# Kernel optimization log

Hardware: AMD Instinct MI355X
Metric: run time of the kernel (lower is better)

The kernel has to match this reference:

```python
import jax, jax.numpy as jnp
import numpy as np

K = 5       # kernel_size
NV = 12     # number of orientation vectors
CIN = 8
COUT = 8

ICO = np.array([[-0.525731, 0.850651, 0.0], [0.525731, 0.850651, 0.0],
                [-0.525731, -0.850651, 0.0], [0.525731, -0.850651, 0.0],
                [0.0, -0.525731, 0.850651], [0.0, 0.525731, 0.850651],
                [0.0, -0.525731, -0.850651], [0.0, 0.525731, -0.850651],
                [0.850651, 0.0, -0.525731], [0.850651, 0.0, 0.525731],
                [-0.850651, 0.0, -0.525731], [-0.850651, 0.0, 0.525731]],
               dtype=np.float32)


def _attrs():
    # invariant_attr_r3s2_fiber_bundle on the fixed k^3 stencil graph
    off = np.arange(K) - K // 2 + (K + 1) % 2 * 0.5
    grid = np.stack(np.meshgrid(off, off, off, indexing='ij'), 0)
    pos = grid.transpose(1, 2, 3, 0).reshape(-1, 3)              # [K^3, 3]
    rel = pos[K ** 3 // 2][None, :] - pos                        # pos_send - pos_receive, [E,3]
    inv1 = (rel[:, None, :] * ICO[None]).sum(-1, keepdims=True)  # [E,NV,1] parallel component
    inv2 = np.linalg.norm(rel[:, None, :] - inv1 * ICO[None], axis=-1, keepdims=True)  # orthogonal norm
    spatial = np.concatenate([inv1, inv2], -1).round(5).reshape(-1, 2)   # rounded as in module
    spherical = (ICO @ ICO.T).round(3).reshape(-1, 1)                     # [NV*NV, 1]
    return jnp.asarray(spatial, jnp.float32), jnp.asarray(spherical, jnp.float32)


def _poly(x, degree=3):
    # PolynomialFeatures: cat of x, x(x)x, x(x)x(x)x flattened
    feats = [x]
    for _ in range(1, degree):
        f = feats[-1][..., :, None] * x[..., None, :]
        feats.append(f.reshape(f.shape[:-2] + (-1,)))
    return jnp.concatenate(feats, -1)


def _mlp(a, w1, b1, w2, b2, w3):
    h = jax.nn.gelu(a @ w1.T + b1, approximate=False)
    h = jax.nn.gelu(h @ w2.T + b2, approximate=False)
    return h @ w3.T


def setup_inputs() -> dict:
    key = jax.random.key(0)
    ks = jax.random.split(key, 8)
    spatial, spherical = _attrs()

    def lin(k, o, i):
        return (jax.random.normal(k, (o, i), jnp.float32) / np.sqrt(i)).astype(jnp.float32)

    return dict(
        x=jax.random.normal(ks[0], (2, CIN, NV, 64, 64, 64), jnp.float32),
        spatial_attr=spatial,            # [1500, 2]
        spherical_attr=spherical,        # [144, 1]
        basis_w1=lin(ks[1], 8, 14), basis_b1=jnp.zeros(8, jnp.float32),
        basis_w2=lin(ks[2], 8, 8),  basis_b2=jnp.zeros(8, jnp.float32),
        basis_w3=lin(ks[3], CIN, 8),
        fiber_w1=lin(ks[4], 8, 3),  fiber_b1=jnp.zeros(8, jnp.float32),
        fiber_w2=lin(ks[5], 8, 8),  fiber_b2=jnp.zeros(8, jnp.float32),
        fiber_w3=lin(ks[6], CIN * COUT, 8),
        bias=jnp.full((1, COUT, 1, 1, 1, 1), 0.01, jnp.float32),
    )


def reference(x, spatial_attr, spherical_attr,
              basis_w1, basis_b1, basis_w2, basis_b2, basis_w3,
              fiber_w1, fiber_b1, fiber_w2, fiber_b2, fiber_w3, bias):
    # Spatial (depthwise) kernel generated by tiny MLP on edge invariants.
    # (Original uniques attrs then gathers; basis(unique)[inverse] == basis(attr), so apply directly.)
    sw = _mlp(_poly(spatial_attr), basis_w1, basis_b1, basis_w2, basis_b2, basis_w3)  # [K^3*NV, CIN]
    sw = sw.reshape(K, K, K, NV, CIN).transpose(4, 3, 0, 1, 2).reshape(CIN * NV, 1, K, K, K)
    # Fiber (orientation-mixing) weights from MLP on orientation invariants.
    fw = _mlp(_poly(spherical_attr), fiber_w1, fiber_b1, fiber_w2, fiber_b2, fiber_w3)  # [NV*NV, CIN*COUT]
    fw = fw.reshape(NV, NV, CIN, COUT).transpose(3, 2, 0, 1)  # [COUT, CIN, NV, NV]

    B, _, _, X, Y, Z = x.shape
    xr = x.reshape(B, CIN * NV, X, Y, Z)
    y = jax.lax.conv_general_dilated(
        xr, sw, window_strides=(1, 1, 1), padding='SAME',
        feature_group_count=CIN * NV,
        dimension_numbers=('NCDHW', 'OIDHW', 'NCDHW'))
    y = y.reshape(B, CIN, NV, X, Y, Z)
    out = jnp.einsum('bfvxyz,gfvw->bgwxyz', y, fw)
    return out + bias
```

## Files before the change

### kernel.cpp

```cpp
#include <hip/hip_runtime.h>
#include <math.h>

#define DEV __device__ __forceinline__

DEV float gelu_exact(float v) {
    return 0.5f * v * (1.0f + erff(v * 0.7071067811865476f));
}

typedef __attribute__((ext_vector_type(8))) short bf16x8;
typedef __attribute__((ext_vector_type(4))) float f32x4;

DEV short f2b(float f) {
    unsigned u = __builtin_bit_cast(unsigned, f);
    unsigned r = (u + 0x7fffu + ((u >> 16) & 1u)) >> 16;
    return (short)r;
}

__global__ __launch_bounds__(256) void wk(
    const float* __restrict__ spatial, const float* __restrict__ spherical,
    const float* __restrict__ bw1, const float* __restrict__ bb1,
    const float* __restrict__ bw2, const float* __restrict__ bb2,
    const float* __restrict__ bw3,
    const float* __restrict__ fw1, const float* __restrict__ fb1,
    const float* __restrict__ fw2, const float* __restrict__ fb2,
    const float* __restrict__ fw3,
    float* __restrict__ sw, float* __restrict__ Mt) {
    const int i = blockIdx.x * 256 + threadIdx.x;
    if (i < 1500) {
        const float a = spatial[2 * i], b = spatial[2 * i + 1];
        float ft[14];
        ft[0] = a; ft[1] = b;
        ft[2] = a * a; ft[3] = a * b; ft[4] = b * a; ft[5] = b * b;
#pragma unroll
        for (int k = 0; k < 4; ++k) {
            ft[6 + 2 * k] = ft[2 + k] * a;
            ft[7 + 2 * k] = ft[2 + k] * b;
        }
        float h1[8], h2[8];
#pragma unroll
        for (int j = 0; j < 8; ++j) {
            float s = bb1[j];
#pragma unroll
            for (int k = 0; k < 14; ++k) s = fmaf(bw1[j * 14 + k], ft[k], s);
            h1[j] = gelu_exact(s);
        }
#pragma unroll
        for (int j = 0; j < 8; ++j) {
            float s = bb2[j];
#pragma unroll
            for (int k = 0; k < 8; ++k) s = fmaf(bw2[j * 8 + k], h1[k], s);
            h2[j] = gelu_exact(s);
        }
        const int o = i / 12, v = i % 12;
#pragma unroll
        for (int c = 0; c < 8; ++c) {
            float s = 0.f;
#pragma unroll
            for (int k = 0; k < 8; ++k) s = fmaf(bw3[c * 8 + k], h2[k], s);
            sw[(c * 12 + v) * 125 + o] = s;
        }
    } else if (i < 1644) {
        const int r = i - 1500;
        const float s0 = spherical[r];
        float ft[3];
        ft[0] = s0; ft[1] = s0 * s0; ft[2] = s0 * s0 * s0;
        float h1[8], h2[8];
#pragma unroll
        for (int j = 0; j < 8; ++j) {
            float s = fb1[j];
#pragma unroll
            for (int k = 0; k < 3; ++k) s = fmaf(fw1[j * 3 + k], ft[k], s);
            h1[j] = gelu_exact(s);
        }
#pragma unroll
        for (int j = 0; j < 8; ++j) {
            float s = fb2[j];
#pragma unroll
            for (int k = 0; k < 8; ++k) s = fmaf(fw2[j * 8 + k], h1[k], s);
            h2[j] = gelu_exact(s);
        }
        const int v = r / 12, w = r % 12;
#pragma unroll
        for (int c = 0; c < 64; ++c) {
            float s = 0.f;
#pragma unroll
            for (int k = 0; k < 8; ++k) s = fmaf(fw3[c * 8 + k], h2[k], s);
            const int f = c >> 3, g = c & 7;
            Mt[(f * 12 + v) * 96 + g * 12 + w] = s;
        }
    }
}

__global__ __launch_bounds__(256) void ck(const float* __restrict__ x,
                                          const float* __restrict__ sw,
                                          float* __restrict__ y) {
    const int ch = blockIdx.y, b = blockIdx.z;
    const int ty = (blockIdx.x & 7) << 3;
    const int tz = (blockIdx.x >> 3) << 3;
    const int t = threadIdx.x;
    const int xq = t & 15, x0 = xq << 2;
    const int y0 = ty + (((t >> 4) & 3) << 1);
    const int z0 = tz + ((t >> 6) << 1);
    const long cb = (long)(b * 96 + ch) << 18;
    const float* __restrict__ xb = x + cb;
    float* __restrict__ yb = y + cb;
    const float* __restrict__ w = sw + ch * 125;

    float acc[2][2][4];
#pragma unroll
    for (int i = 0; i < 2; ++i)
#pragma unroll
        for (int j = 0; j < 2; ++j)
#pragma unroll
            for (int k = 0; k < 4; ++k) acc[i][j][k] = 0.f;

#pragma unroll
    for (int hz = 0; hz < 6; ++hz) {
        const int zz = z0 + hz - 2;
        if (zz < 0 || zz >= 64) continue;
#pragma unroll
        for (int hy = 0; hy < 6; ++hy) {
            const int yy = y0 + hy - 2;
            if (yy >= 0 && yy < 64) {
                const float* row = xb + (zz << 12) + (yy << 6);
                const float4 v4 = *(const float4*)(row + x0);
                const float uz = __shfl_up(v4.z, 1, 16);
                const float uw = __shfl_up(v4.w, 1, 16);
                const float dx_ = __shfl_down(v4.x, 1, 16);
                const float dy_ = __shfl_down(v4.y, 1, 16);
                float f[8];
                f[0] = (xq > 0) ? uz : 0.f;
                f[1] = (xq > 0) ? uw : 0.f;
                f[2] = v4.x; f[3] = v4.y; f[4] = v4.z; f[5] = v4.w;
                f[6] = (xq < 15) ? dx_ : 0.f;
                f[7] = (xq < 15) ? dy_ : 0.f;
#pragma unroll
                for (int dz = 0; dz < 2; ++dz) {
                    const int A = hz - dz;
                    if (A < 0 || A > 4) continue;
#pragma unroll
                    for (int dy = 0; dy < 2; ++dy) {
                        const int B = hy - dy;
                        if (B < 0 || B > 4) continue;
                        const float* wr = w + (A * 5 + B) * 5;
#pragma unroll
                        for (int C = 0; C < 5; ++C) {
                            const float wv = wr[C];
#pragma unroll
                            for (int dx = 0; dx < 4; ++dx)
                                acc[dz][dy][dx] = fmaf(f[C + dx], wv, acc[dz][dy][dx]);
                        }
                    }
                }
            }
        }
    }
#pragma unroll
    for (int dz = 0; dz < 2; ++dz)
#pragma unroll
        for (int dy = 0; dy < 2; ++dy) {
            float4 o;
            o.x = acc[dz][dy][0]; o.y = acc[dz][dy][1];
            o.z = acc[dz][dy][2]; o.w = acc[dz][dy][3];
            *(float4*)(yb + ((z0 + dz) << 12) + ((y0 + dy) << 6) + x0) = o;
        }
}

__global__ __launch_bounds__(256) void ek(float* __restrict__ io,
                                          const float* __restrict__ Mt,
                                          const float* __restrict__ bias) {
    const int t = threadIdx.x;
    const int lane = t & 63;
    const int wv = t >> 6;
    const int l15 = lane & 15, quad = lane >> 4;
    const long b_off = ((long)blockIdx.y * 96) << 18;
    const int pt0 = (blockIdx.x << 7) + (wv << 5);

    bf16x8 Af[6][3];
#pragma unroll
    for (int mt = 0; mt < 6; ++mt)
#pragma unroll
        for (int ks = 0; ks < 3; ++ks)
#pragma unroll
            for (int j = 0; j < 8; ++j) {
                const int fv = ks * 32 + quad * 8 + j;
                Af[mt][ks][j] = f2b(Mt[fv * 96 + mt * 16 + l15]);
            }

    bf16x8 Bf[2][3];
#pragma unroll
    for (int nt = 0; nt < 2; ++nt)
#pragma unroll
        for (int ks = 0; ks < 3; ++ks)
#pragma unroll
            for (int j = 0; j < 8; ++j) {
                const int fv = ks * 32 + quad * 8 + j;
                Bf[nt][ks][j] = f2b(io[b_off + ((long)fv << 18) + pt0 + nt * 16 + l15]);
            }

#pragma unroll
    for (int mt = 0; mt < 6; ++mt)
#pragma unroll
        for (int nt = 0; nt < 2; ++nt) {
            f32x4 c = {0.f, 0.f, 0.f, 0.f};
#pragma unroll
            for (int ks = 0; ks < 3; ++ks)
                c = __builtin_amdgcn_mfma_f32_16x16x32_bf16(Af[mt][ks], Bf[nt][ks], c, 0, 0, 0);
#pragma unroll
            for (int r = 0; r < 4; ++r) {
                const int gw = mt * 16 + quad * 4 + r;
                io[b_off + ((long)gw << 18) + pt0 + nt * 16 + l15] = c[r] + bias[gw / 12];
            }
        }
}

extern "C" void kernel_launch(void* const* d_in, const int* in_sizes, int n_in,
                              void* d_out, int out_size, void* d_ws, size_t ws_size,
                              hipStream_t stream) {
    const float* x        = (const float*)d_in[0];
    const float* spatial  = (const float*)d_in[1];
    const float* spherical= (const float*)d_in[2];
    const float* bw1 = (const float*)d_in[3];
    const float* bb1 = (const float*)d_in[4];
    const float* bw2 = (const float*)d_in[5];
    const float* bb2 = (const float*)d_in[6];
    const float* bw3 = (const float*)d_in[7];
    const float* fw1 = (const float*)d_in[8];
    const float* fb1 = (const float*)d_in[9];
    const float* fw2 = (const float*)d_in[10];
    const float* fb2 = (const float*)d_in[11];
    const float* fw3 = (const float*)d_in[12];
    const float* bias = (const float*)d_in[13];

    float* sw = (float*)d_ws;
    float* Mt = (float*)d_ws + 12032;
    float* out = (float*)d_out;

    hipLaunchKernelGGL(wk, dim3(7), dim3(256), 0, stream,
                       spatial, spherical, bw1, bb1, bw2, bb2, bw3,
                       fw1, fb1, fw2, fb2, fw3, sw, Mt);
    hipLaunchKernelGGL(ck, dim3(64, 96, 2), dim3(256), 0, stream, x, sw, out);
    hipLaunchKernelGGL(ek, dim3(2048, 2, 1), dim3(256), 0, stream, out, Mt, bias);
    (void)in_sizes; (void)n_in; (void)out_size; (void)ws_size;
}
```

Measured before the change: 623.2 us.

## Stage conv halo tile and einsum input in LDS, pre-pack bf16 fiber weights

The depthwise conv kernel now loads a 12x12-row halo tile into shared memory with zero padding and an XOR swizzle. Each thread then computes 8 x-outputs across 2 y rows from LDS, replacing the repeated global loads and cross-lane shuffles. The einsum kernel first stages its 96x128 input slice in LDS with coalesced float4 loads. The fiber weight matrix is pre-transposed and pre-converted to bf16 in the weight kernel, so A fragments become single vector loads per mt. The cost is larger LDS use per block, which may lower occupancy.

```diff
diff --git a/kernel.cpp b/kernel.cpp
--- a/kernel.cpp
+++ b/kernel.cpp
@@ -24,7 +24,7 @@
     const float* __restrict__ fw1, const float* __restrict__ fb1,
     const float* __restrict__ fw2, const float* __restrict__ fb2,
     const float* __restrict__ fw3,
-    float* __restrict__ sw, float* __restrict__ Mt) {
+    float* __restrict__ sw, unsigned short* __restrict__ Mtt) {
     const int i = blockIdx.x * 256 + threadIdx.x;
     if (i < 1500) {
         const float a = spatial[2 * i], b = spatial[2 * i + 1];
@@ -86,132 +86,163 @@
 #pragma unroll
             for (int k = 0; k < 8; ++k) s = fmaf(fw3[c * 8 + k], h2[k], s);
             const int f = c >> 3, g = c & 7;
-            Mt[(f * 12 + v) * 96 + g * 12 + w] = s;
-        }
-    }
-}
-
+            Mtt[(g * 12 + w) * 96 + f * 12 + v] = (unsigned short)f2b(s);
+        }
+    }
+}
+
+#define CPITCH 80
 __global__ __launch_bounds__(256) void ck(const float* __restrict__ x,
                                           const float* __restrict__ sw,
                                           float* __restrict__ y) {
+    __shared__ float lds[12 * 12 * CPITCH];
     const int ch = blockIdx.y, b = blockIdx.z;
     const int ty = (blockIdx.x & 7) << 3;
     const int tz = (blockIdx.x >> 3) << 3;
     const int t = threadIdx.x;
-    const int xq = t & 15, x0 = xq << 2;
-    const int y0 = ty + (((t >> 4) & 3) << 1);
-    const int z0 = tz + ((t >> 6) << 1);
     const long cb = (long)(b * 96 + ch) << 18;
     const float* __restrict__ xb = x + cb;
     float* __restrict__ yb = y + cb;
     const float* __restrict__ w = sw + ch * 125;
 
-    float acc[2][2][4];
+    {
+        const int l16 = t & 15;
+        const int rq = t >> 4;
+#pragma unroll
+        for (int pass = 0; pass < 9; ++pass) {
+            const int r = rq + (pass << 4);
+            const int zi = r / 12, yi = r % 12;
+            const int zz = tz + zi - 2, yy = ty + yi - 2;
+            float4 v = {0.f, 0.f, 0.f, 0.f};
+            if (zz >= 0 && zz < 64 && yy >= 0 && yy < 64)
+                v = *(const float4*)(xb + (zz << 12) + (yy << 6) + (l16 << 2));
+            const int s = (r >> 2) & 3;
+            float* rp = lds + r * CPITCH;
+            float* p0 = rp + (((l16 ^ s) << 2) + 2);
+            p0[0] = v.x; p0[1] = v.y;
+            float* p1 = rp + (((l16 + 1) ^ s) << 2);
+            p1[0] = v.z; p1[1] = v.w;
+            if (l16 == 0) {
+                float* p = rp + ((0 ^ s) << 2);
+                p[0] = 0.f; p[1] = 0.f;
+            }
+            if (l16 == 15) {
+                float* p = rp + (((16 ^ s) << 2) + 2);
+                p[0] = 0.f; p[1] = 0.f;
+            }
+        }
+    }
+    __syncthreads();
+
+    const int xg = t & 7;
+    const int yg = (t >> 3) & 3;
+    const int zg = t >> 5;
+    const int w0 = xg << 1;
+
+    float acc[2][8];
 #pragma unroll
     for (int i = 0; i < 2; ++i)
 #pragma unroll
-        for (int j = 0; j < 2; ++j)
-#pragma unroll
-            for (int k = 0; k < 4; ++k) acc[i][j][k] = 0.f;
-
-#pragma unroll
-    for (int hz = 0; hz < 6; ++hz) {
-        const int zz = z0 + hz - 2;
-        if (zz < 0 || zz >= 64) continue;
+        for (int j = 0; j < 8; ++j) acc[i][j] = 0.f;
+
+#pragma unroll
+    for (int hz = 0; hz < 5; ++hz) {
 #pragma unroll
         for (int hy = 0; hy < 6; ++hy) {
-            const int yy = y0 + hy - 2;
-            if (yy >= 0 && yy < 64) {
-                const float* row = xb + (zz << 12) + (yy << 6);
-                const float4 v4 = *(const float4*)(row + x0);
-                const float uz = __shfl_up(v4.z, 1, 16);
-                const float uw = __shfl_up(v4.w, 1, 16);
-                const float dx_ = __shfl_down(v4.x, 1, 16);
-                const float dy_ = __shfl_down(v4.y, 1, 16);
-                float f[8];
-                f[0] = (xq > 0) ? uz : 0.f;
-                f[1] = (xq > 0) ? uw : 0.f;
-                f[2] = v4.x; f[3] = v4.y; f[4] = v4.z; f[5] = v4.w;
-                f[6] = (xq < 15) ? dx_ : 0.f;
-                f[7] = (xq < 15) ? dy_ : 0.f;
-#pragma unroll
-                for (int dz = 0; dz < 2; ++dz) {
-                    const int A = hz - dz;
-                    if (A < 0 || A > 4) continue;
-#pragma unroll
-                    for (int dy = 0; dy < 2; ++dy) {
-                        const int B = hy - dy;
-                        if (B < 0 || B > 4) continue;
-                        const float* wr = w + (A * 5 + B) * 5;
-#pragma unroll
-                        for (int C = 0; C < 5; ++C) {
-                            const float wv = wr[C];
-#pragma unroll
-                            for (int dx = 0; dx < 4; ++dx)
-                                acc[dz][dy][dx] = fmaf(f[C + dx], wv, acc[dz][dy][dx]);
-                        }
-                    }
+            const int row = (zg + hz) * 12 + (yg << 1) + hy;
+            const int s = (row >> 2) & 3;
+            const float* rp = lds + row * CPITCH;
+            const float4 fa = *(const float4*)(rp + (((w0 + 0) ^ s) << 2));
+            const float4 fb = *(const float4*)(rp + (((w0 + 1) ^ s) << 2));
+            const float4 fc = *(const float4*)(rp + (((w0 + 2) ^ s) << 2));
+            const float f[12] = {fa.x, fa.y, fa.z, fa.w, fb.x, fb.y, fb.z, fb.w,
+                                 fc.x, fc.y, fc.z, fc.w};
+#pragma unroll
+            for (int dy = 0; dy < 2; ++dy) {
+                const int B = hy - dy;
+                if (B < 0 || B > 4) continue;
+                const float* wr = w + (hz * 5 + B) * 5;
+#pragma unroll
+                for (int C = 0; C < 5; ++C) {
+                    const float wv = wr[C];
+#pragma unroll
+                    for (int dx = 0; dx < 8; ++dx)
+                        acc[dy][dx] = fmaf(f[C + dx], wv, acc[dy][dx]);
                 }
             }
         }
     }
-#pragma unroll
-    for (int dz = 0; dz < 2; ++dz)
-#pragma unroll
-        for (int dy = 0; dy < 2; ++dy) {
-            float4 o;
-            o.x = acc[dz][dy][0]; o.y = acc[dz][dy][1];
-            o.z = acc[dz][dy][2]; o.w = acc[dz][dy][3];
-            *(float4*)(yb + ((z0 + dz) << 12) + ((y0 + dy) << 6) + x0) = o;
-        }
-}
-
+
+    const int zo = tz + zg;
+    const int xo = xg << 3;
+#pragma unroll
+    for (int dy = 0; dy < 2; ++dy) {
+        const int yo = ty + (yg << 1) + dy;
+        float* op = yb + (zo << 12) + (yo << 6) + xo;
+        float4 o0 = {acc[dy][0], acc[dy][1], acc[dy][2], acc[dy][3]};
+        float4 o1 = {acc[dy][4], acc[dy][5], acc[dy][6], acc[dy][7]};
+        *(float4*)(op) = o0;
+        *(float4*)(op + 4) = o1;
+    }
+}
+
+#define EPITCH 132
 __global__ __launch_bounds__(256) void ek(float* __restrict__ io,
-                                          const float* __restrict__ Mt,
+                                          const unsigned short* __restrict__ Mtt,
                                           const float* __restrict__ bias) {
+    __shared__ float yt[96 * EPITCH];
     const int t = threadIdx.x;
+    const long b_off = ((long)blockIdx.y * 96) << 18;
+    const int pt0 = blockIdx.x << 7;
+
+    {
+        const int l32 = t & 31;
+        const int r8 = t >> 5;
+#pragma unroll
+        for (int pass = 0; pass < 12; ++pass) {
+            const int fv = r8 + (pass << 3);
+            const float4 v = *(const float4*)(io + b_off + ((long)fv << 18) + pt0 + (l32 << 2));
+            *(float4*)(yt + fv * EPITCH + (l32 << 2)) = v;
+        }
+    }
+    __syncthreads();
+
     const int lane = t & 63;
     const int wv = t >> 6;
     const int l15 = lane & 15, quad = lane >> 4;
-    const long b_off = ((long)blockIdx.y * 96) << 18;
-    const int pt0 = (blockIdx.x << 7) + (wv << 5);
-
-    bf16x8 Af[6][3];
-#pragma unroll
-    for (int mt = 0; mt < 6; ++mt)
+    const int ptl = wv << 5;
+
+    bf16x8 Bf[2][3];
+#pragma unroll
+    for (int nt = 0; nt < 2; ++nt)
 #pragma unroll
         for (int ks = 0; ks < 3; ++ks)
 #pragma unroll
             for (int j = 0; j < 8; ++j) {
                 const int fv = ks * 32 + quad * 8 + j;
-                Af[mt][ks][j] = f2b(Mt[fv * 96 + mt * 16 + l15]);
-            }
-
-    bf16x8 Bf[2][3];
-#pragma unroll
-    for (int nt = 0; nt < 2; ++nt)
+                Bf[nt][ks][j] = f2b(yt[fv * EPITCH + ptl + nt * 16 + l15]);
+            }
+
+    const long po = b_off + pt0 + ptl;
+#pragma unroll
+    for (int mt = 0; mt < 6; ++mt) {
+        bf16x8 Af[3];
 #pragma unroll
         for (int ks = 0; ks < 3; ++ks)
-#pragma unroll
-            for (int j = 0; j < 8; ++j) {
-                const int fv = ks * 32 + quad * 8 + j;
-                Bf[nt][ks][j] = f2b(io[b_off + ((long)fv << 18) + pt0 + nt * 16 + l15]);
-            }
-
-#pragma unroll
-    for (int mt = 0; mt < 6; ++mt)
+            Af[ks] = *(const bf16x8*)(Mtt + (mt * 16 + l15) * 96 + ks * 32 + quad * 8);
 #pragma unroll
         for (int nt = 0; nt < 2; ++nt) {
             f32x4 c = {0.f, 0.f, 0.f, 0.f};
 #pragma unroll
             for (int ks = 0; ks < 3; ++ks)
-                c = __builtin_amdgcn_mfma_f32_16x16x32_bf16(Af[mt][ks], Bf[nt][ks], c, 0, 0, 0);
+                c = __builtin_amdgcn_mfma_f32_16x16x32_bf16(Af[ks], Bf[nt][ks], c, 0, 0, 0);
 #pragma unroll
             for (int r = 0; r < 4; ++r) {
                 const int gw = mt * 16 + quad * 4 + r;
-                io[b_off + ((long)gw << 18) + pt0 + nt * 16 + l15] = c[r] + bias[gw / 12];
-            }
-        }
+                io[po + ((long)gw << 18) + nt * 16 + l15] = c[r] + bias[gw / 12];
+            }
+        }
+    }
 }
 
 extern "C" void kernel_launch(void* const* d_in, const int* in_sizes, int n_in,
@@ -233,13 +264,13 @@
     const float* bias = (const float*)d_in[13];
 
     float* sw = (float*)d_ws;
-    float* Mt = (float*)d_ws + 12032;
+    unsigned short* Mtt = (unsigned short*)((char*)d_ws + 48128);
     float* out = (float*)d_out;
 
     hipLaunchKernelGGL(wk, dim3(7), dim3(256), 0, stream,
                        spatial, spherical, bw1, bb1, bw2, bb2, bw3,
-                       fw1, fb1, fw2, fb2, fw3, sw, Mt);
+                       fw1, fb1, fw2, fb2, fw3, sw, Mtt);
     hipLaunchKernelGGL(ck, dim3(64, 96, 2), dim3(256), 0, stream, x, sw, out);
-    hipLaunchKernelGGL(ek, dim3(2048, 2, 1), dim3(256), 0, stream, out, Mt, bias);
+    hipLaunchKernelGGL(ek, dim3(2048, 2, 1), dim3(256), 0, stream, out, Mtt, bias);
     (void)in_sizes; (void)n_in; (void)out_size; (void)ws_size;
 }
```

Result: faster. 587.1 us (-5.8%).

## Store conv intermediate as packed bf16 and stage mixing GEMM through LDS

Applied to the files above, without the earlier changes.

The depthwise conv kernel now handles two channels per thread and writes its result as packed bf16 pairs instead of fp32. This halves the intermediate write and read traffic. The mixing kernel loads these packed rows into swizzled LDS with coalesced 16-byte accesses, builds the MFMA B fragments from LDS, and writes output through LDS so global stores are fully coalesced. The fiber weights are precomputed as transposed bf16, so the mixing kernel loads A fragments as vectors instead of converting scalars per element. It adds LDS use and barriers, and relies on in-place reuse of the output buffer.

```diff
diff --git a/kernel.cpp b/kernel.cpp
--- a/kernel.cpp
+++ b/kernel.cpp
@@ -24,7 +24,7 @@
     const float* __restrict__ fw1, const float* __restrict__ fb1,
     const float* __restrict__ fw2, const float* __restrict__ fb2,
     const float* __restrict__ fw3,
-    float* __restrict__ sw, float* __restrict__ Mt) {
+    float* __restrict__ sw, unsigned short* __restrict__ Mtt) {
     const int i = blockIdx.x * 256 + threadIdx.x;
     if (i < 1500) {
         const float a = spatial[2 * i], b = spatial[2 * i + 1];
@@ -86,132 +86,193 @@
 #pragma unroll
             for (int k = 0; k < 8; ++k) s = fmaf(fw3[c * 8 + k], h2[k], s);
             const int f = c >> 3, g = c & 7;
-            Mt[(f * 12 + v) * 96 + g * 12 + w] = s;
+            Mtt[(g * 12 + w) * 96 + f * 12 + v] = (unsigned short)f2b(s);
         }
     }
 }
 
 __global__ __launch_bounds__(256) void ck(const float* __restrict__ x,
                                           const float* __restrict__ sw,
-                                          float* __restrict__ y) {
-    const int ch = blockIdx.y, b = blockIdx.z;
+                                          unsigned int* __restrict__ yp) {
+    const int chp = blockIdx.y, b = blockIdx.z;
     const int ty = (blockIdx.x & 7) << 3;
     const int tz = (blockIdx.x >> 3) << 3;
     const int t = threadIdx.x;
     const int xq = t & 15, x0 = xq << 2;
     const int y0 = ty + (((t >> 4) & 3) << 1);
     const int z0 = tz + ((t >> 6) << 1);
-    const long cb = (long)(b * 96 + ch) << 18;
-    const float* __restrict__ xb = x + cb;
-    float* __restrict__ yb = y + cb;
-    const float* __restrict__ w = sw + ch * 125;
-
-    float acc[2][2][4];
-#pragma unroll
-    for (int i = 0; i < 2; ++i)
-#pragma unroll
-        for (int j = 0; j < 2; ++j)
-#pragma unroll
-            for (int k = 0; k < 4; ++k) acc[i][j][k] = 0.f;
-
-#pragma unroll
-    for (int hz = 0; hz < 6; ++hz) {
-        const int zz = z0 + hz - 2;
-        if (zz < 0 || zz >= 64) continue;
-#pragma unroll
-        for (int hy = 0; hy < 6; ++hy) {
-            const int yy = y0 + hy - 2;
-            if (yy >= 0 && yy < 64) {
-                const float* row = xb + (zz << 12) + (yy << 6);
-                const float4 v4 = *(const float4*)(row + x0);
-                const float uz = __shfl_up(v4.z, 1, 16);
-                const float uw = __shfl_up(v4.w, 1, 16);
-                const float dx_ = __shfl_down(v4.x, 1, 16);
-                const float dy_ = __shfl_down(v4.y, 1, 16);
-                float f[8];
-                f[0] = (xq > 0) ? uz : 0.f;
-                f[1] = (xq > 0) ? uw : 0.f;
-                f[2] = v4.x; f[3] = v4.y; f[4] = v4.z; f[5] = v4.w;
-                f[6] = (xq < 15) ? dx_ : 0.f;
-                f[7] = (xq < 15) ? dy_ : 0.f;
-#pragma unroll
-                for (int dz = 0; dz < 2; ++dz) {
-                    const int A = hz - dz;
-                    if (A < 0 || A > 4) continue;
-#pragma unroll
-                    for (int dy = 0; dy < 2; ++dy) {
-                        const int B = hy - dy;
-                        if (B < 0 || B > 4) continue;
-                        const float* wr = w + (A * 5 + B) * 5;
-#pragma unroll
-                        for (int C = 0; C < 5; ++C) {
-                            const float wv = wr[C];
-#pragma unroll
-                            for (int dx = 0; dx < 4; ++dx)
-                                acc[dz][dy][dx] = fmaf(f[C + dx], wv, acc[dz][dy][dx]);
+
+    unsigned int pk[2][2][4];
+
+#pragma unroll
+    for (int c2 = 0; c2 < 2; ++c2) {
+        const int ch = 2 * chp + c2;
+        const float* __restrict__ xb = x + ((long)(b * 96 + ch) << 18);
+        const float* __restrict__ w = sw + ch * 125;
+
+        float acc[2][2][4];
+#pragma unroll
+        for (int i = 0; i < 2; ++i)
+#pragma unroll
+            for (int j = 0; j < 2; ++j)
+#pragma unroll
+                for (int k = 0; k < 4; ++k) acc[i][j][k] = 0.f;
+
+#pragma unroll
+        for (int hz = 0; hz < 6; ++hz) {
+            const int zz = z0 + hz - 2;
+            if (zz < 0 || zz >= 64) continue;
+#pragma unroll
+            for (int hy = 0; hy < 6; ++hy) {
+                const int yy = y0 + hy - 2;
+                if (yy >= 0 && yy < 64) {
+                    const float* row = xb + (zz << 12) + (yy << 6);
+                    const float4 v4 = *(const float4*)(row + x0);
+                    const float uz = __shfl_up(v4.z, 1, 16);
+                    const float uw = __shfl_up(v4.w, 1, 16);
+                    const float dx_ = __shfl_down(v4.x, 1, 16);
+                    const float dy_ = __shfl_down(v4.y, 1, 16);
+                    float f[8];
+                    f[0] = (xq > 0) ? uz : 0.f;
+                    f[1] = (xq > 0) ? uw : 0.f;
+                    f[2] = v4.x; f[3] = v4.y; f[4] = v4.z; f[5] = v4.w;
+                    f[6] = (xq < 15) ? dx_ : 0.f;
+                    f[7] = (xq < 15) ? dy_ : 0.f;
+#pragma unroll
+                    for (int dz = 0; dz < 2; ++dz) {
+                        const int A = hz - dz;
+                        if (A < 0 || A > 4) continue;
+#pragma unroll
+                        for (int dy = 0; dy < 2; ++dy) {
+                            const int B = hy - dy;
+                            if (B < 0 || B > 4) continue;
+                            const float* wr = w + (A * 5 + B) * 5;
+#pragma unroll
+                            for (int C = 0; C < 5; ++C) {
+                                const float wv = wr[C];
+#pragma unroll
+                                for (int dx = 0; dx < 4; ++dx)
+                                    acc[dz][dy][dx] = fmaf(f[C + dx], wv, acc[dz][dy][dx]);
+                            }
                         }
                     }
                 }
             }
         }
-    }
+#pragma unroll
+        for (int dz = 0; dz < 2; ++dz)
+#pragma unroll
+            for (int dy = 0; dy < 2; ++dy)
+#pragma unroll
+                for (int dx = 0; dx < 4; ++dx) {
+                    const unsigned int h = (unsigned short)f2b(acc[dz][dy][dx]);
+                    if (c2 == 0) pk[dz][dy][dx] = h;
+                    else         pk[dz][dy][dx] |= (h << 16);
+                }
+    }
+
+    unsigned int* yb = yp + ((long)(b * 96 + chp) << 18);
 #pragma unroll
     for (int dz = 0; dz < 2; ++dz)
 #pragma unroll
         for (int dy = 0; dy < 2; ++dy) {
-            float4 o;
-            o.x = acc[dz][dy][0]; o.y = acc[dz][dy][1];
-            o.z = acc[dz][dy][2]; o.w = acc[dz][dy][3];
-            *(float4*)(yb + ((z0 + dz) << 12) + ((y0 + dy) << 6) + x0) = o;
+            uint4 o;
+            o.x = pk[dz][dy][0]; o.y = pk[dz][dy][1];
+            o.z = pk[dz][dy][2]; o.w = pk[dz][dy][3];
+            *(uint4*)(yb + ((z0 + dz) << 12) + ((y0 + dy) << 6) + x0) = o;
         }
 }
 
 __global__ __launch_bounds__(256) void ek(float* __restrict__ io,
-                                          const float* __restrict__ Mt,
+                                          const unsigned int* __restrict__ yp,
+                                          const unsigned short* __restrict__ Mtt,
                                           const float* __restrict__ bias) {
+    __shared__ float lds[96 * 128];
+    unsigned int* ldu = (unsigned int*)lds;
     const int t = threadIdx.x;
+    const long row0 = (long)blockIdx.y * 96;
+    const int pt0 = blockIdx.x << 7;
+
+    {
+        const int l32 = t & 31, r8 = t >> 5;
+#pragma unroll
+        for (int pass = 0; pass < 6; ++pass) {
+            const int pr = r8 + (pass << 3);
+            const uint4 v = *(const uint4*)(yp + ((row0 + pr) << 18) + pt0 + (l32 << 2));
+            const int ws = (l32 + pr) & 31;
+            *(uint4*)(ldu + (pr << 7) + (ws << 2)) = v;
+        }
+    }
+    __syncthreads();
+
     const int lane = t & 63;
-    const int wv = t >> 6;
+    const int wv4 = t >> 6;
     const int l15 = lane & 15, quad = lane >> 4;
-    const long b_off = ((long)blockIdx.y * 96) << 18;
-    const int pt0 = (blockIdx.x << 7) + (wv << 5);
-
-    bf16x8 Af[6][3];
-#pragma unroll
-    for (int mt = 0; mt < 6; ++mt)
+    const int ptl = wv4 << 5;
+
+    bf16x8 Bf[2][3];
+#pragma unroll
+    for (int nt = 0; nt < 2; ++nt)
+#pragma unroll
+        for (int ks = 0; ks < 3; ++ks) {
+            const int pt = ptl + nt * 16 + l15;
+            const int pr0 = 16 * ks + 4 * quad;
+            uint4 d;
+            {
+                const int b0 = (pt >> 2) + pr0;
+                d.x = ldu[((pr0 + 0) << 7) + (((b0 + 0) & 31) << 2) + (pt & 3)];
+                d.y = ldu[((pr0 + 1) << 7) + (((b0 + 1) & 31) << 2) + (pt & 3)];
+                d.z = ldu[((pr0 + 2) << 7) + (((b0 + 2) & 31) << 2) + (pt & 3)];
+                d.w = ldu[((pr0 + 3) << 7) + (((b0 + 3) & 31) << 2) + (pt & 3)];
+            }
+            Bf[nt][ks] = __builtin_bit_cast(bf16x8, d);
+        }
+
+    float cv[6][2][4];
+#pragma unroll
+    for (int mt = 0; mt < 6; ++mt) {
+        bf16x8 Af[3];
 #pragma unroll
         for (int ks = 0; ks < 3; ++ks)
-#pragma unroll
-            for (int j = 0; j < 8; ++j) {
-                const int fv = ks * 32 + quad * 8 + j;
-                Af[mt][ks][j] = f2b(Mt[fv * 96 + mt * 16 + l15]);
-            }
-
-    bf16x8 Bf[2][3];
-#pragma unroll
-    for (int nt = 0; nt < 2; ++nt)
-#pragma unroll
-        for (int ks = 0; ks < 3; ++ks)
-#pragma unroll
-            for (int j = 0; j < 8; ++j) {
-                const int fv = ks * 32 + quad * 8 + j;
-                Bf[nt][ks][j] = f2b(io[b_off + ((long)fv << 18) + pt0 + nt * 16 + l15]);
-            }
-
-#pragma unroll
-    for (int mt = 0; mt < 6; ++mt)
+            Af[ks] = *(const bf16x8*)(Mtt + (mt * 16 + l15) * 96 + ks * 32 + quad * 8);
 #pragma unroll
         for (int nt = 0; nt < 2; ++nt) {
             f32x4 c = {0.f, 0.f, 0.f, 0.f};
 #pragma unroll
             for (int ks = 0; ks < 3; ++ks)
-                c = __builtin_amdgcn_mfma_f32_16x16x32_bf16(Af[mt][ks], Bf[nt][ks], c, 0, 0, 0);
+                c = __builtin_amdgcn_mfma_f32_16x16x32_bf16(Af[ks], Bf[nt][ks], c, 0, 0, 0);
+#pragma unroll
+            for (int r = 0; r < 4; ++r) cv[mt][nt][r] = c[r];
+        }
+    }
+    __syncthreads();
+
+#pragma unroll
+    for (int mt = 0; mt < 6; ++mt)
+#pragma unroll
+        for (int nt = 0; nt < 2; ++nt) {
+            const int pt = ptl + nt * 16 + l15;
 #pragma unroll
             for (int r = 0; r < 4; ++r) {
                 const int gw = mt * 16 + quad * 4 + r;
-                io[b_off + ((long)gw << 18) + pt0 + nt * 16 + l15] = c[r] + bias[gw / 12];
+                const int ws = ((pt >> 2) + 2 * (gw >> 2)) & 31;
+                lds[(gw << 7) + (ws << 2) + (pt & 3)] = cv[mt][nt][r];
             }
         }
+    __syncthreads();
+
+    {
+        const int l32 = t & 31, r8 = t >> 5;
+#pragma unroll
+        for (int pass = 0; pass < 12; ++pass) {
+            const int row = r8 + (pass << 3);
+            const int ws = (l32 + 2 * (row >> 2)) & 31;
+            float4 v = *(const float4*)(lds + (row << 7) + (ws << 2));
+            const float bs = bias[row / 12];
+            v.x += bs; v.y += bs; v.z += bs; v.w += bs;
+            *(float4*)(io + ((row0 + row) << 18) + pt0 + (l32 << 2)) = v;
+        }
+    }
 }
 
 extern "C" void kernel_launch(void* const* d_in, const int* in_sizes, int n_in,
@@ -233,13 +294,15 @@
     const float* bias = (const float*)d_in[13];
 
     float* sw = (float*)d_ws;
-    float* Mt = (float*)d_ws + 12032;
+    unsigned short* Mtt = (unsigned short*)((char*)d_ws + 48128);
     float* out = (float*)d_out;
 
     hipLaunchKernelGGL(wk, dim3(7), dim3(256), 0, stream,
                        spatial, spherical, bw1, bb1, bw2, bb2, bw3,
-                       fw1, fb1, fw2, fb2, fw3, sw, Mt);
-    hipLaunchKernelGGL(ck, dim3(64, 96, 2), dim3(256), 0, stream, x, sw, out);
-    hipLaunchKernelGGL(ek, dim3(2048, 2, 1), dim3(256), 0, stream, out, Mt, bias);
+                       fw1, fb1, fw2, fb2, fw3, sw, Mtt);
+    hipLaunchKernelGGL(ck, dim3(64, 48, 2), dim3(256), 0, stream,
+                       x, sw, (unsigned int*)out);
+    hipLaunchKernelGGL(ek, dim3(2048, 2, 1), dim3(256), 0, stream,
+                       out, (const unsigned int*)out, Mtt, bias);
     (void)in_sizes; (void)n_in; (void)out_size; (void)ws_size;
 }
```

Measured after the change: 581.9 us. 1.07x faster.

## Fuse depthwise conv and fiber-mixing MFMA into one kernel via LDS

Applied to the files above, without the earlier changes.

The depthwise 5x5x5 conv and the orientation-mixing GEMM are merged into one kernel. Each block computes conv outputs for all 96 channels of a 4-row tile, packs them as bf16 into swizzled shared memory, and then runs the MFMA mixing directly from LDS. The fiber weights are also precomputed as transposed bf16 so they load as vectors. This removes the full fp32 intermediate round trip through global memory. In exchange each thread computes only 4 outputs per channel, so halo reloads of x increase (25 rows per output row instead of sharing across a 2x2 tile), and LDS use limits occupancy.

```diff
diff --git a/kernel.cpp b/kernel.cpp
--- a/kernel.cpp
+++ b/kernel.cpp
@@ -15,6 +15,8 @@
     unsigned r = (u + 0x7fffu + ((u >> 16) & 1u)) >> 16;
     return (short)r;
 }
+
+DEV int rmap(int pt) { return pt ^ ((pt >> 2) & 7); }
 
 __global__ __launch_bounds__(256) void wk(
     const float* __restrict__ spatial, const float* __restrict__ spherical,
@@ -24,7 +26,7 @@
     const float* __restrict__ fw1, const float* __restrict__ fb1,
     const float* __restrict__ fw2, const float* __restrict__ fb2,
     const float* __restrict__ fw3,
-    float* __restrict__ sw, float* __restrict__ Mt) {
+    float* __restrict__ sw, unsigned short* __restrict__ Mtt) {
     const int i = blockIdx.x * 256 + threadIdx.x;
     if (i < 1500) {
         const float a = spatial[2 * i], b = spatial[2 * i + 1];
@@ -86,44 +88,60 @@
 #pragma unroll
             for (int k = 0; k < 8; ++k) s = fmaf(fw3[c * 8 + k], h2[k], s);
             const int f = c >> 3, g = c & 7;
-            Mt[(f * 12 + v) * 96 + g * 12 + w] = s;
-        }
-    }
-}
-
-__global__ __launch_bounds__(256) void ck(const float* __restrict__ x,
+            Mtt[(g * 12 + w) * 96 + f * 12 + v] = (unsigned short)f2b(s);
+        }
+    }
+}
+
+__global__ __launch_bounds__(256) void fk(const float* __restrict__ x,
                                           const float* __restrict__ sw,
-                                          float* __restrict__ y) {
-    const int ch = blockIdx.y, b = blockIdx.z;
-    const int ty = (blockIdx.x & 7) << 3;
-    const int tz = (blockIdx.x >> 3) << 3;
+                                          const unsigned short* __restrict__ Mtt,
+                                          const float* __restrict__ bias,
+                                          float* __restrict__ out) {
+    __shared__ __align__(16) unsigned short yt[256 * 104];
     const int t = threadIdx.x;
-    const int xq = t & 15, x0 = xq << 2;
-    const int y0 = ty + (((t >> 4) & 3) << 1);
-    const int z0 = tz + ((t >> 6) << 1);
-    const long cb = (long)(b * 96 + ch) << 18;
-    const float* __restrict__ xb = x + cb;
-    float* __restrict__ yb = y + cb;
-    const float* __restrict__ w = sw + ch * 125;
-
-    float acc[2][2][4];
-#pragma unroll
-    for (int i = 0; i < 2; ++i)
-#pragma unroll
-        for (int j = 0; j < 2; ++j)
-#pragma unroll
-            for (int k = 0; k < 4; ++k) acc[i][j][k] = 0.f;
-
-#pragma unroll
-    for (int hz = 0; hz < 6; ++hz) {
-        const int zz = z0 + hz - 2;
-        if (zz < 0 || zz >= 64) continue;
-#pragma unroll
-        for (int hy = 0; hy < 6; ++hy) {
-            const int yy = y0 + hy - 2;
-            if (yy >= 0 && yy < 64) {
-                const float* row = xb + (zz << 12) + (yy << 6);
-                const float4 v4 = *(const float4*)(row + x0);
+    const int b = blockIdx.y;
+    const int bx = blockIdx.x;
+    const int cid = bx >> 2;
+    const int yti = ((cid & 15) << 1) | (bx & 1);
+    const int zti = ((cid >> 4) << 1) | ((bx >> 1) & 1);
+    const int ty = yti << 1, tz = zti << 1;
+
+    const int xq = t & 15;
+    const int g = (t >> 4) & 3;
+    const int zg = g >> 1, yg = g & 1;
+    const int wvu = __builtin_amdgcn_readfirstlane(t >> 6);
+
+    int off[25];
+    unsigned vm = 0;
+#pragma unroll
+    for (int r = 0; r < 25; ++r) {
+        const int hz = r / 5, hy = r % 5;
+        const int zz = tz + zg + hz - 2;
+        const int yy = ty + yg + hy - 2;
+        const int zc = min(max(zz, 0), 63), yc = min(max(yy, 0), 63);
+        off[r] = (zc << 12) + (yc << 6) + (xq << 2);
+        if ((unsigned)zz < 64u && (unsigned)yy < 64u) vm |= (1u << r);
+    }
+
+    unsigned* const ytw = (unsigned*)yt;
+#pragma unroll 1
+    for (int itp = 0; itp < 12; ++itp) {
+        unsigned pk[4];
+#pragma unroll
+        for (int c2 = 0; c2 < 2; ++c2) {
+            const int ch = wvu * 24 + itp * 2 + c2;
+            const float* __restrict__ xb = x + ((long)(b * 96 + ch) << 18);
+            const float* __restrict__ w = sw + ch * 125;
+            float acc[4] = {0.f, 0.f, 0.f, 0.f};
+#pragma unroll
+            for (int r = 0; r < 25; ++r) {
+                float4 v4 = *(const float4*)(xb + off[r]);
+                const bool ok = (vm >> r) & 1u;
+                v4.x = ok ? v4.x : 0.f;
+                v4.y = ok ? v4.y : 0.f;
+                v4.z = ok ? v4.z : 0.f;
+                v4.w = ok ? v4.w : 0.f;
                 const float uz = __shfl_up(v4.z, 1, 16);
                 const float uw = __shfl_up(v4.w, 1, 16);
                 const float dx_ = __shfl_down(v4.x, 1, 16);
@@ -134,84 +152,64 @@
                 f[2] = v4.x; f[3] = v4.y; f[4] = v4.z; f[5] = v4.w;
                 f[6] = (xq < 15) ? dx_ : 0.f;
                 f[7] = (xq < 15) ? dy_ : 0.f;
-#pragma unroll
-                for (int dz = 0; dz < 2; ++dz) {
-                    const int A = hz - dz;
-                    if (A < 0 || A > 4) continue;
-#pragma unroll
-                    for (int dy = 0; dy < 2; ++dy) {
-                        const int B = hy - dy;
-                        if (B < 0 || B > 4) continue;
-                        const float* wr = w + (A * 5 + B) * 5;
-#pragma unroll
-                        for (int C = 0; C < 5; ++C) {
-                            const float wv = wr[C];
-#pragma unroll
-                            for (int dx = 0; dx < 4; ++dx)
-                                acc[dz][dy][dx] = fmaf(f[C + dx], wv, acc[dz][dy][dx]);
-                        }
-                    }
+                const float* wr = w + r * 5;
+#pragma unroll
+                for (int C = 0; C < 5; ++C) {
+                    const float wv_ = wr[C];
+#pragma unroll
+                    for (int dx = 0; dx < 4; ++dx)
+                        acc[dx] = fmaf(f[C + dx], wv_, acc[dx]);
                 }
             }
-        }
-    }
-#pragma unroll
-    for (int dz = 0; dz < 2; ++dz)
-#pragma unroll
-        for (int dy = 0; dy < 2; ++dy) {
-            float4 o;
-            o.x = acc[dz][dy][0]; o.y = acc[dz][dy][1];
-            o.z = acc[dz][dy][2]; o.w = acc[dz][dy][3];
-            *(float4*)(yb + ((z0 + dz) << 12) + ((y0 + dy) << 6) + x0) = o;
-        }
-}
-
-__global__ __launch_bounds__(256) void ek(float* __restrict__ io,
-                                          const float* __restrict__ Mt,
-                                          const float* __restrict__ bias) {
-    const int t = threadIdx.x;
+#pragma unroll
+            for (int dx = 0; dx < 4; ++dx) {
+                const unsigned h = (unsigned short)f2b(acc[dx]);
+                if (c2 == 0) pk[dx] = h;
+                else         pk[dx] |= (h << 16);
+            }
+        }
+        const int col = wvu * 12 + itp;
+#pragma unroll
+        for (int dx = 0; dx < 4; ++dx) {
+            const int pt = (g << 6) + (xq << 2) + dx;
+            ytw[rmap(pt) * 52 + col] = pk[dx];
+        }
+    }
+    __syncthreads();
+
     const int lane = t & 63;
-    const int wv = t >> 6;
     const int l15 = lane & 15, quad = lane >> 4;
-    const long b_off = ((long)blockIdx.y * 96) << 18;
-    const int pt0 = (blockIdx.x << 7) + (wv << 5);
-
-    bf16x8 Af[6][3];
-#pragma unroll
-    for (int mt = 0; mt < 6; ++mt)
+
+    bf16x8 Bf[4][3];
+#pragma unroll
+    for (int kk = 0; kk < 4; ++kk)
+#pragma unroll
+        for (int ks = 0; ks < 3; ++ks) {
+            const int pt = (wvu << 6) + (kk << 4) + l15;
+            Bf[kk][ks] = *(const bf16x8*)(yt + rmap(pt) * 104 + ks * 32 + quad * 8);
+        }
+
+    const long ob = ((long)b * 96) << 18;
+    const int ptg0 = ((tz + (wvu >> 1)) << 12) + ((ty + (wvu & 1)) << 6);
+#pragma unroll
+    for (int mt = 0; mt < 6; ++mt) {
+        bf16x8 Af[3];
 #pragma unroll
         for (int ks = 0; ks < 3; ++ks)
-#pragma unroll
-            for (int j = 0; j < 8; ++j) {
-                const int fv = ks * 32 + quad * 8 + j;
-                Af[mt][ks][j] = f2b(Mt[fv * 96 + mt * 16 + l15]);
-            }
-
-    bf16x8 Bf[2][3];
-#pragma unroll
-    for (int nt = 0; nt < 2; ++nt)
-#pragma unroll
-        for (int ks = 0; ks < 3; ++ks)
-#pragma unroll
-            for (int j = 0; j < 8; ++j) {
-                const int fv = ks * 32 + quad * 8 + j;
-                Bf[nt][ks][j] = f2b(io[b_off + ((long)fv << 18) + pt0 + nt * 16 + l15]);
-            }
-
-#pragma unroll
-    for (int mt = 0; mt < 6; ++mt)
-#pragma unroll
-        for (int nt = 0; nt < 2; ++nt) {
+            Af[ks] = *(const bf16x8*)(Mtt + (mt * 16 + l15) * 96 + ks * 32 + quad * 8);
+#pragma unroll
+        for (int kk = 0; kk < 4; ++kk) {
             f32x4 c = {0.f, 0.f, 0.f, 0.f};
 #pragma unroll
             for (int ks = 0; ks < 3; ++ks)
-                c = __builtin_amdgcn_mfma_f32_16x16x32_bf16(Af[mt][ks], Bf[nt][ks], c, 0, 0, 0);
+                c = __builtin_amdgcn_mfma_f32_16x16x32_bf16(Af[ks], Bf[kk][ks], c, 0, 0, 0);
 #pragma unroll
             for (int r = 0; r < 4; ++r) {
                 const int gw = mt * 16 + quad * 4 + r;
-                io[b_off + ((long)gw << 18) + pt0 + nt * 16 + l15] = c[r] + bias[gw / 12];
+                out[ob + ((long)gw << 18) + ptg0 + (kk << 4) + l15] = c[r] + bias[gw / 12];
             }
         }
+    }
 }
 
 extern "C" void kernel_launch(void* const* d_in, const int* in_sizes, int n_in,
@@ -233,13 +231,13 @@
     const float* bias = (const float*)d_in[13];
 
     float* sw = (float*)d_ws;
-    float* Mt = (float*)d_ws + 12032;
+    unsigned short* Mtt = (unsigned short*)((char*)d_ws + 48128);
     float* out = (float*)d_out;
 
     hipLaunchKernelGGL(wk, dim3(7), dim3(256), 0, stream,
                        spatial, spherical, bw1, bb1, bw2, bb2, bw3,
-                       fw1, fb1, fw2, fb2, fw3, sw, Mt);
-    hipLaunchKernelGGL(ck, dim3(64, 96, 2), dim3(256), 0, stream, x, sw, out);
-    hipLaunchKernelGGL(ek, dim3(2048, 2, 1), dim3(256), 0, stream, out, Mt, bias);
+                       fw1, fb1, fw2, fb2, fw3, sw, Mtt);
+    hipLaunchKernelGGL(fk, dim3(1024, 2), dim3(256), 0, stream,
+                       x, sw, Mtt, bias, out);
     (void)in_sizes; (void)n_in; (void)out_size; (void)ws_size;
 }
```

Result: slower. 704.6 us (+13.1%).
